# Optimization experiments

Hardware: AMD Instinct MI355X
Metric: run time of the kernel (lower is better)

Reference implementation:

```python
import jax, jax.numpy as jnp
import numpy as np
import math

D_MODEL = 1024
NUM_HEADS = 16
D_K = D_MODEL // NUM_HEADS
THETA = 10000.0
BATCH = 2
SEQ = 2048


def setup_inputs() -> dict:
    key = jax.random.key(0)
    k = jax.random.split(key, 6)
    scale = 1.0 / math.sqrt(D_MODEL)
    in_features = jax.random.normal(k[0], (BATCH, SEQ, D_MODEL), dtype=jnp.float32)
    token_positions = jnp.sort(
        jax.random.randint(k[1], (BATCH, SEQ), 0, SEQ), axis=-1
    ).astype(jnp.int32)
    q_proj_weight = jax.random.normal(k[2], (D_MODEL, D_MODEL), dtype=jnp.float32) * scale
    k_proj_weight = jax.random.normal(k[3], (D_MODEL, D_MODEL), dtype=jnp.float32) * scale
    v_proj_weight = jax.random.normal(k[4], (D_MODEL, D_MODEL), dtype=jnp.float32) * scale
    o_proj_weight = jax.random.normal(k[5], (D_MODEL, D_MODEL), dtype=jnp.float32) * scale
    return {
        "in_features": in_features,
        "token_positions": token_positions,
        "q_proj_weight": q_proj_weight,
        "k_proj_weight": k_proj_weight,
        "v_proj_weight": v_proj_weight,
        "o_proj_weight": o_proj_weight,
    }


def _apply_rope(x, positions):
    # x: [b, h, s, d_k]; positions: [b, s]
    freqs = 1.0 / (THETA ** (jnp.arange(0, D_K, 2, dtype=jnp.float32) / D_K))  # [d_k/2]
    angles = positions[:, None, :, None].astype(jnp.float32) * freqs  # [b,1,s,d_k/2]
    cos, sin = jnp.cos(angles), jnp.sin(angles)
    x1 = x[..., 0::2]
    x2 = x[..., 1::2]
    x1r = x1 * cos - x2 * sin
    x2r = x1 * sin + x2 * cos
    # interleave pairs back: stack on new last axis then flatten
    return jnp.stack([x1r, x2r], axis=-1).reshape(x.shape)


def reference(in_features, token_positions, q_proj_weight, k_proj_weight,
              v_proj_weight, o_proj_weight):
    b, s, _ = in_features.shape
    Q = jnp.einsum('bsi,di->bsd', in_features, q_proj_weight)
    K = jnp.einsum('bsi,di->bsd', in_features, k_proj_weight)
    V = jnp.einsum('bsi,di->bsd', in_features, v_proj_weight)
    # split heads: [b, h, s, d_k]
    def split(x):
        return x.reshape(b, s, NUM_HEADS, D_K).transpose(0, 2, 1, 3)
    Q, K, V = split(Q), split(K), split(V)
    Q = _apply_rope(Q, token_positions)
    K = _apply_rope(K, token_positions)
    scores = jnp.einsum('bhqd,bhkd->bhqk', Q, K) / math.sqrt(D_K)
    causal = jnp.tril(jnp.ones((s, s), dtype=bool))  # allowed positions
    scores = jnp.where(causal[None, None], scores, -jnp.inf)
    weights = jax.nn.softmax(scores, axis=-1)
    head_out = jnp.einsum('bhqk,bhkd->bhqd', weights, V)
    combined = head_out.transpose(0, 2, 1, 3).reshape(b, s, D_MODEL)
    return jnp.einsum('bsd,od->bso', combined, o_proj_weight)
```

## Files before the change

kernel.cpp:

```cpp
#include <hip/hip_runtime.h>
#include <hip/hip_bf16.h>
#include <stdint.h>

#define DMODEL 1024
#define NH 16
#define DKH 64
#define BB 2
#define SS 2048
#define MTOT (BB*SS)

#define BK 32
#define TP 136

using f32x4  = __attribute__((ext_vector_type(4))) float;
using bf16x8 = __attribute__((ext_vector_type(8))) __bf16;

#define GLL(g, l) __builtin_amdgcn_global_load_lds( \
    (const __attribute__((address_space(1))) unsigned int*)(g), \
    (__attribute__((address_space(3))) unsigned int*)(l), 16, 0, 0)

__device__ __forceinline__ unsigned short f2bf(float f) {
  union { float f; uint32_t u; } v; v.f = f;
  uint32_t r = v.u + 0x7FFFu + ((v.u >> 16) & 1u);
  return (unsigned short)(r >> 16);
}

__global__ __launch_bounds__(256) void cvt_all(
    const float* __restrict__ X,
    const float* __restrict__ w0, const float* __restrict__ w1,
    const float* __restrict__ w2, const float* __restrict__ w3,
    unsigned short* __restrict__ Xb,
    unsigned short* __restrict__ Wb)
{
  const int bid = blockIdx.x;
  const float* src;
  unsigned short* dst;
  int i;
  if (bid < 2048) {
    src = X; dst = Xb; i = bid * 256 + threadIdx.x;
  } else {
    int t = bid - 2048;
    int z = t >> 9;
    src = (z == 0) ? w0 : (z == 1) ? w1 : (z == 2) ? w2 : w3;
    dst = Wb + (size_t)z * DMODEL * DMODEL;
    i = (t & 511) * 256 + threadIdx.x;
  }
  const float4* s4 = (const float4*)src;
  float4 a = s4[2*i], b = s4[2*i+1];
  uint4 o;
  o.x = (uint32_t)f2bf(a.x) | ((uint32_t)f2bf(a.y) << 16);
  o.y = (uint32_t)f2bf(a.z) | ((uint32_t)f2bf(a.w) << 16);
  o.z = (uint32_t)f2bf(b.x) | ((uint32_t)f2bf(b.y) << 16);
  o.w = (uint32_t)f2bf(b.z) | ((uint32_t)f2bf(b.w) << 16);
  *(uint4*)(dst + (size_t)i * 8) = o;
}

template<int MI, int NI>
__device__ __forceinline__ void gemm_pipe(
    const unsigned short* __restrict__ A,
    const unsigned short* __restrict__ Bw,
    int m0, int n0, int K,
    unsigned short* As, unsigned short* Bs,
    f32x4 (&acc)[MI][NI])
{
  const int BMl = MI * 32;
  const int BNl = NI * 32;
  const int tid = threadIdx.x;
  const int lane = tid & 63;
  const int w = tid >> 6;
  const int wr = w >> 1, wc = w & 1;
  const int lrow = lane & 15;
  const int g = lane >> 4;

  const f32x4 fzero = {0.f, 0.f, 0.f, 0.f};
  #pragma unroll
  for (int i = 0; i < MI; ++i)
    #pragma unroll
    for (int j = 0; j < NI; ++j)
      acc[i][j] = fzero;

  const int nk = K / BK;

  const unsigned short* aSrc[MI / 2];
  const unsigned short* bSrc[NI / 2];
  int aLds[MI / 2], bLds[NI / 2];
  #pragma unroll
  for (int c = 0; c < MI / 2; ++c) {
    int i = tid + c * 256;
    int row = i >> 2, cc = i & 3;
    int sc = cc ^ ((row >> 1) & 3);
    aSrc[c] = A + (size_t)(m0 + row) * K + sc * 8;
    aLds[c] = i * 8;
  }
  #pragma unroll
  for (int c = 0; c < NI / 2; ++c) {
    int i = tid + c * 256;
    int row = i >> 2, cc = i & 3;
    int sc = cc ^ ((row >> 1) & 3);
    bSrc[c] = Bw + (size_t)(n0 + row) * K + sc * 8;
    bLds[c] = i * 8;
  }
  int aOff[MI], bOff[NI];
  #pragma unroll
  for (int mi = 0; mi < MI; ++mi) {
    int row = wr * (MI * 16) + mi * 16 + lrow;
    aOff[mi] = row * BK + (g ^ ((row >> 1) & 3)) * 8;
  }
  #pragma unroll
  for (int ni = 0; ni < NI; ++ni) {
    int row = wc * (NI * 16) + ni * 16 + lrow;
    bOff[ni] = row * BK + (g ^ ((row >> 1) & 3)) * 8;
  }

  auto STAGE = [&](int k0, int buf) {
    #pragma unroll
    for (int c = 0; c < MI / 2; ++c)
      GLL(aSrc[c] + k0, As + buf * (BMl * BK) + aLds[c]);
    #pragma unroll
    for (int c = 0; c < NI / 2; ++c)
      GLL(bSrc[c] + k0, Bs + buf * (BNl * BK) + bLds[c]);
  };

  STAGE(0, 0);
  __syncthreads();
  for (int t = 0; t < nk; ++t) {
    const int cur = t & 1;
    if (t + 1 < nk) STAGE((t + 1) * BK, cur ^ 1);

    const unsigned short* Ab = As + cur * (BMl * BK);
    const unsigned short* Bb = Bs + cur * (BNl * BK);
    bf16x8 af[MI], bfr[NI];
    #pragma unroll
    for (int mi = 0; mi < MI; ++mi)
      af[mi] = *(const bf16x8*)(Ab + aOff[mi]);
    #pragma unroll
    for (int ni = 0; ni < NI; ++ni)
      bfr[ni] = *(const bf16x8*)(Bb + bOff[ni]);
    #pragma unroll
    for (int mi = 0; mi < MI; ++mi)
      #pragma unroll
      for (int ni = 0; ni < NI; ++ni)
        acc[mi][ni] = __builtin_amdgcn_mfma_f32_16x16x32_bf16(af[mi], bfr[ni], acc[mi][ni], 0, 0, 0);

    __syncthreads();
  }
}

__global__ __launch_bounds__(256) void gemm_qkv(
    const unsigned short* __restrict__ Xb,
    const unsigned short* __restrict__ Wf,
    const int* __restrict__ tpos,
    unsigned short* __restrict__ Qh,
    unsigned short* __restrict__ Kh,
    unsigned short* __restrict__ Vt)
{
  __shared__ __align__(16) unsigned char smraw[128 * TP * 2];
  unsigned short* sm = (unsigned short*)smraw;
  unsigned short* As = sm;
  unsigned short* Bs = sm + 2 * 128 * BK;

  const int m0 = blockIdx.x * 128;
  const int n0 = blockIdx.y * 128;
  const int z  = n0 >> 10;
  const int nloc = n0 & 1023;

  f32x4 acc[4][4];
  gemm_pipe<4, 4>(Xb, Wf, m0, n0, DMODEL, As, Bs, acc);

  const int tid  = threadIdx.x;
  const int lane = tid & 63;
  const int w    = tid >> 6;
  const int wr   = w >> 1, wc = w & 1;
  const int cb   = lane & 15, rb = (lane >> 4) * 4;

  if (z < 2) {
    #pragma unroll
    for (int mi = 0; mi < 4; ++mi)
      #pragma unroll
      for (int ni = 0; ni < 4; ++ni)
        #pragma unroll
        for (int r = 0; r < 4; ++r)
          sm[(wr * 64 + mi * 16 + rb + r) * TP + wc * 64 + ni * 16 + cb] = f2bf(acc[mi][ni][r]);
  } else {
    #pragma unroll
    for (int mi = 0; mi < 4; ++mi)
      #pragma unroll
      for (int ni = 0; ni < 4; ++ni)
        #pragma unroll
        for (int r = 0; r < 4; ++r)
          sm[(wc * 64 + ni * 16 + cb) * TP + wr * 64 + mi * 16 + rb + r] = f2bf(acc[mi][ni][r]);
  }
  __syncthreads();

  const int b = m0 >> 11;
  const float l2t = 13.28771237954945f / 32.0f;
  const float qsc = (z == 0) ? 0.18033688011112042f : 1.0f;

  if (z < 2) {
    unsigned short* dst = (z == 0) ? Qh : Kh;
    #pragma unroll
    for (int p = 0; p < 8; ++p) {
      const int m_l = p * 16 + (tid >> 4);
      const int ck  = tid & 15;
      bf16x8 vals = *(const bf16x8*)(sm + m_l * TP + ck * 8);
      const int m = m0 + m_l, s = m & (SS - 1);
      const int pos = tpos[m];
      const int n = nloc + ck * 8, h = n >> 6, dh = n & 63;
      union { unsigned short u[8]; uint4 v; } ov;
      #pragma unroll
      for (int e = 0; e < 4; ++e) {
        float x1 = (float)vals[2 * e], x2 = (float)vals[2 * e + 1];
        int j = (dh >> 1) + e;
        float ang = (float)pos * exp2f(-(float)j * l2t);
        float sn, cs;
        __sincosf(ang, &sn, &cs);
        sn *= qsc; cs *= qsc;
        ov.u[2 * e]     = f2bf(x1 * cs - x2 * sn);
        ov.u[2 * e + 1] = f2bf(x1 * sn + x2 * cs);
      }
      *(uint4*)(dst + ((size_t)(b * NH + h) * SS + s) * DKH + dh) = ov.v;
    }
  } else {
    #pragma unroll
    for (int p = 0; p < 8; ++p) {
      const int n_l = p * 16 + (tid >> 4);
      const int ck  = tid & 15;
      bf16x8 vals = *(const bf16x8*)(sm + n_l * TP + ck * 8);
      const int n = nloc + n_l, h = n >> 6, dh = n & 63;
      const int m = m0 + ck * 8, s = m & (SS - 1);
      *(bf16x8*)(Vt + ((size_t)(b * NH + h) * DKH + dh) * SS + s) = vals;
    }
  }
}

__global__ __launch_bounds__(256) void attn(
    const unsigned short* __restrict__ Qh,
    const unsigned short* __restrict__ Kh,
    const unsigned short* __restrict__ Vt,
    unsigned short* __restrict__ comb)
{
  __shared__ unsigned short Ks[2][128 * 64];
  __shared__ unsigned short Vs[2][64 * 128];
  __shared__ unsigned short Ps[4][32 * 64];

  const int idx = blockIdx.x;
  const int x = idx & 7;
  const int o = idx >> 3;
  const int bh = x * 4 + (o & 3);
  const int j = o >> 2;
  const int qt = (j < 8) ? j : 23 - j;

  const int tid = threadIdx.x, lane = tid & 63, w = tid >> 6;
  const int lc = lane & 15, lh = lane >> 4;

  const unsigned short* kb = Kh + (size_t)bh * SS * DKH;
  const unsigned short* vb = Vt + (size_t)bh * DKH * SS;
  const int b = bh >> 4, h = bh & 15;
  const f32x4 fzero = {0.f, 0.f, 0.f, 0.f};
  const int Q0 = qt * 128;

  auto STAGE = [&](int t, int buf) {
    const int kv0 = t * 128;
    #pragma unroll
    for (int c = 0; c < 4; ++c) {
      int i = tid + c * 256;
      int row = i >> 3, pc = i & 7;
      int sc = pc ^ (row & 7);
      GLL(kb + (size_t)(kv0 + row) * DKH + sc * 8, &Ks[buf][i * 8]);
    }
    #pragma unroll
    for (int c = 0; c < 4; ++c) {
      int i = tid + c * 256;
      int row = i >> 4, cc = i & 15;
      int sc = cc ^ (row & 7);
      GLL(vb + (size_t)row * SS + kv0 + sc * 8, &Vs[buf][i * 8]);
    }
  };

  bf16x8 qf[2][2];
  #pragma unroll
  for (int qg = 0; qg < 2; ++qg) {
    const unsigned short* Qb = Qh + ((size_t)bh * SS + Q0 + w * 32 + qg * 16 + lc) * DKH;
    qf[qg][0] = *(const bf16x8*)(Qb + lh * 8);
    qf[qg][1] = *(const bf16x8*)(Qb + lh * 8 + 32);
  }

  f32x4 oacc[2][4];
  #pragma unroll
  for (int qg = 0; qg < 2; ++qg)
    #pragma unroll
    for (int i = 0; i < 4; ++i) oacc[qg][i] = fzero;
  float lsum[2] = {0.f, 0.f};
  unsigned short* psw = &Ps[w][0];

  auto QK = [&](int cur, int hh, f32x4 (&sacc)[2][4]) {
    __builtin_amdgcn_s_setprio(1);
    #pragma unroll
    for (int nf = 0; nf < 4; ++nf) {
      const int row = hh * 64 + nf * 16 + lc;
      bf16x8 kf0 = *(const bf16x8*)(&Ks[cur][row * 64 + ((lh) ^ (row & 7)) * 8]);
      bf16x8 kf1 = *(const bf16x8*)(&Ks[cur][row * 64 + ((lh + 4) ^ (row & 7)) * 8]);
      #pragma unroll
      for (int qg = 0; qg < 2; ++qg) {
        sacc[qg][nf] = __builtin_amdgcn_mfma_f32_16x16x32_bf16(kf0, qf[qg][0], fzero, 0, 0, 0);
        sacc[qg][nf] = __builtin_amdgcn_mfma_f32_16x16x32_bf16(kf1, qf[qg][1], sacc[qg][nf], 0, 0, 0);
      }
    }
    __builtin_amdgcn_s_setprio(0);
  };

  auto SM = [&](f32x4 (&sacc)[2][4], bool domask, int t, int hh) {
    #pragma unroll
    for (int qg = 0; qg < 2; ++qg) {
      float sv[4][4];
      if (domask) {
        const int kv0 = t * 128 + hh * 64;
        const int qlane = Q0 + w * 32 + qg * 16 + lc;
        #pragma unroll
        for (int nf = 0; nf < 4; ++nf)
          #pragma unroll
          for (int r = 0; r < 4; ++r) {
            float x2 = sacc[qg][nf][r];
            if ((kv0 + nf * 16 + lh * 4 + r) > qlane) x2 = -1e30f;
            sv[nf][r] = x2;
          }
      } else {
        #pragma unroll
        for (int nf = 0; nf < 4; ++nf)
          #pragma unroll
          for (int r = 0; r < 4; ++r)
            sv[nf][r] = sacc[qg][nf][r];
      }
      float rs = 0.f;
      #pragma unroll
      for (int nf = 0; nf < 4; ++nf)
        #pragma unroll
        for (int r = 0; r < 4; ++r) {
          float p = exp2f(sv[nf][r]);
          sv[nf][r] = p;
          rs += p;
        }
      lsum[qg] += rs;
      #pragma unroll
      for (int nf = 0; nf < 4; ++nf) {
        uint32_t u0, u1;
        asm("v_cvt_pk_bf16_f32 %0, %1, %2" : "=v"(u0) : "v"(sv[nf][0]), "v"(sv[nf][1]));
        asm("v_cvt_pk_bf16_f32 %0, %1, %2" : "=v"(u1) : "v"(sv[nf][2]), "v"(sv[nf][3]));
        int swz = (nf * 2 + (lh >> 1)) ^ (lc & 7);
        uint32_t* p = (uint32_t*)&psw[(qg * 16 + lc) * 64 + swz * 8 + (lh & 1) * 4];
        p[0] = u0; p[1] = u1;
      }
    }
  };

  auto PV = [&](int cur, int hh) {
    __builtin_amdgcn_s_setprio(1);
    #pragma unroll
    for (int c = 0; c < 2; ++c) {
      bf16x8 pf[2];
      #pragma unroll
      for (int qg = 0; qg < 2; ++qg)
        pf[qg] = *(const bf16x8*)(&psw[(qg * 16 + lc) * 64 + ((c * 4 + lh) ^ (lc & 7)) * 8]);
      #pragma unroll
      for (int df = 0; df < 4; ++df) {
        const int row = df * 16 + lc;
        bf16x8 vf = *(const bf16x8*)(&Vs[cur][row * 128 + ((hh * 8 + c * 4 + lh) ^ (row & 7)) * 8]);
        #pragma unroll
        for (int qg = 0; qg < 2; ++qg)
          oacc[qg][df] = __builtin_amdgcn_mfma_f32_16x16x32_bf16(pf[qg], vf, oacc[qg][df], 0, 0, 0);
      }
    }
    __builtin_amdgcn_s_setprio(0);
  };

  STAGE(0, 0);
  for (int t = 0; t < qt; ++t) {
    const int cur = t & 1;
    asm volatile("s_waitcnt vmcnt(0)" ::: "memory");
    __builtin_amdgcn_s_barrier();
    f32x4 sacc[2][4];
    QK(cur, 0, sacc);
    STAGE(t + 1, cur ^ 1);
    SM(sacc, false, t, 0);
    PV(cur, 0);
    QK(cur, 1, sacc);
    SM(sacc, false, t, 1);
    PV(cur, 1);
  }
  {
    const int cur = qt & 1;
    asm volatile("s_waitcnt vmcnt(0)" ::: "memory");
    __builtin_amdgcn_s_barrier();
    f32x4 sacc[2][4];
    QK(cur, 0, sacc);
    SM(sacc, true, qt, 0);
    PV(cur, 0);
    QK(cur, 1, sacc);
    SM(sacc, true, qt, 1);
    PV(cur, 1);
  }

  #pragma unroll
  for (int qg = 0; qg < 2; ++qg) {
    float ls0 = lsum[qg];
    ls0 += __shfl_xor(ls0, 16);
    ls0 += __shfl_xor(ls0, 32);
    #pragma unroll
    for (int r = 0; r < 4; ++r) {
      float ls = __shfl(ls0, lh * 4 + r);
      float inv = 1.f / ls;
      const int q = Q0 + w * 32 + qg * 16 + lh * 4 + r;
      #pragma unroll
      for (int df = 0; df < 4; ++df) {
        const int d = h * 64 + df * 16 + lc;
        comb[((size_t)(b * SS + q)) * DMODEL + d] = f2bf(oacc[qg][df][r] * inv);
      }
    }
  }
}

__global__ __launch_bounds__(256) void gemm_out(
    const unsigned short* __restrict__ Cb,
    const unsigned short* __restrict__ Wob,
    float* __restrict__ out)
{
  __shared__ __align__(16) unsigned char smraw[128 * TP * 2];
  unsigned short* As = (unsigned short*)smraw;
  unsigned short* Bs = (unsigned short*)smraw + 2 * 128 * BK;
  float* smf = (float*)smraw;

  const int m0 = blockIdx.x * 128, n0 = blockIdx.y * 64;
  f32x4 acc[4][2];
  gemm_pipe<4, 2>(Cb, Wob, m0, n0, DMODEL, As, Bs, acc);

  const int tid  = threadIdx.x;
  const int lane = tid & 63;
  const int w    = tid >> 6;
  const int wr   = w >> 1, wc = w & 1;
  const int cb   = lane & 15, rb = (lane >> 4) * 4;

  #pragma unroll
  for (int mi = 0; mi < 4; ++mi)
    #pragma unroll
    for (int ni = 0; ni < 2; ++ni)
      #pragma unroll
      for (int r = 0; r < 4; ++r)
        smf[(wr * 64 + mi * 16 + rb + r) * 68 + wc * 32 + ni * 16 + cb] = acc[mi][ni][r];
  __syncthreads();

  #pragma unroll
  for (int p = 0; p < 8; ++p) {
    const int row = p * 16 + (tid >> 4);
    const int ck  = tid & 15;
    float4 vv = *(const float4*)(smf + row * 68 + ck * 4);
    *(float4*)(out + (size_t)(m0 + row) * DMODEL + n0 + ck * 4) = vv;
  }
}

extern "C" void kernel_launch(void* const* d_in, const int* in_sizes, int n_in,
                              void* d_out, int out_size, void* d_ws, size_t ws_size,
                              hipStream_t stream) {
  (void)in_sizes; (void)n_in; (void)out_size; (void)ws_size;
  const float* X    = (const float*)d_in[0];
  const int*   tpos = (const int*)d_in[1];
  const float* Wq   = (const float*)d_in[2];
  const float* Wk   = (const float*)d_in[3];
  const float* Wv   = (const float*)d_in[4];
  const float* Wo   = (const float*)d_in[5];
  float* out = (float*)d_out;

  uint8_t* ws = (uint8_t*)d_ws;
  const size_t SZ_X = (size_t)MTOT * DMODEL * 2;
  const size_t SZ_W = (size_t)DMODEL * DMODEL * 2;
  const size_t SZ_H = (size_t)BB * NH * SS * DKH * 2;
  unsigned short* Xb   = (unsigned short*)(ws);
  unsigned short* Wqb  = (unsigned short*)(ws + SZ_X);
  unsigned short* Wob  = (unsigned short*)(ws + SZ_X + 3 * SZ_W);
  unsigned short* Qh   = (unsigned short*)(ws + SZ_X + 4 * SZ_W);
  unsigned short* Kh   = (unsigned short*)(ws + SZ_X + 4 * SZ_W + SZ_H);
  unsigned short* Vt   = (unsigned short*)(ws + SZ_X + 4 * SZ_W + 2 * SZ_H);
  unsigned short* comb = Xb;

  cvt_all<<<dim3(4096), dim3(256), 0, stream>>>(X, Wq, Wk, Wv, Wo, Xb, Wqb);

  gemm_qkv<<<dim3(MTOT / 128, 24), dim3(256), 0, stream>>>(Xb, Wqb, tpos, Qh, Kh, Vt);
  attn<<<dim3(512), dim3(256), 0, stream>>>(Qh, Kh, Vt, comb);
  gemm_out<<<dim3(MTOT / 128, 16), dim3(256), 0, stream>>>(comb, Wob, out);
}
```

Measured before the change: 112.4 us.

## Widen QKV GEMM K-tile to 64 and batch both QK halves before softmax

The shared GEMM pipeline gains a K-unroll template parameter. The QKV projection now stages 64-wide K tiles with a new 8-chunk XOR swizzle, which halves the number of barrier and stage iterations at the cost of 64KB of LDS per block. The attention loop now issues both QK sub-tile MFMAs before the prefetch and softmax instead of interleaving them, giving more independent MFMA work per step. The cost is extra score registers and lower occupancy from the larger LDS footprint.

```diff
diff --git a/kernel.cpp b/kernel.cpp
--- a/kernel.cpp
+++ b/kernel.cpp
@@ -9,7 +9,6 @@
 #define SS 2048
 #define MTOT (BB*SS)
 
-#define BK 32
 #define TP 136
 
 using f32x4  = __attribute__((ext_vector_type(4))) float;
@@ -55,7 +54,7 @@
   *(uint4*)(dst + (size_t)i * 8) = o;
 }
 
-template<int MI, int NI>
+template<int MI, int NI, int KU>
 __device__ __forceinline__ void gemm_pipe(
     const unsigned short* __restrict__ A,
     const unsigned short* __restrict__ Bw,
@@ -63,6 +62,7 @@
     unsigned short* As, unsigned short* Bs,
     f32x4 (&acc)[MI][NI])
 {
+  const int BKT = 32 * KU;
   const int BMl = MI * 32;
   const int BNl = NI * 32;
   const int tid = threadIdx.x;
@@ -79,68 +79,78 @@
     for (int j = 0; j < NI; ++j)
       acc[i][j] = fzero;
 
-  const int nk = K / BK;
-
-  const unsigned short* aSrc[MI / 2];
-  const unsigned short* bSrc[NI / 2];
-  int aLds[MI / 2], bLds[NI / 2];
-  #pragma unroll
-  for (int c = 0; c < MI / 2; ++c) {
+  const int nk = K / BKT;
+
+  const unsigned short* aSrc[(MI * KU) / 2];
+  const unsigned short* bSrc[(NI * KU) / 2];
+  int aLds[(MI * KU) / 2], bLds[(NI * KU) / 2];
+  #pragma unroll
+  for (int c = 0; c < (MI * KU) / 2; ++c) {
     int i = tid + c * 256;
-    int row = i >> 2, cc = i & 3;
-    int sc = cc ^ ((row >> 1) & 3);
+    int row, sc;
+    if constexpr (KU == 1) { row = i >> 2; sc = (i & 3) ^ ((row >> 1) & 3); }
+    else                   { row = i >> 3; sc = (i & 7) ^ (row & 7); }
     aSrc[c] = A + (size_t)(m0 + row) * K + sc * 8;
     aLds[c] = i * 8;
   }
   #pragma unroll
-  for (int c = 0; c < NI / 2; ++c) {
+  for (int c = 0; c < (NI * KU) / 2; ++c) {
     int i = tid + c * 256;
-    int row = i >> 2, cc = i & 3;
-    int sc = cc ^ ((row >> 1) & 3);
+    int row, sc;
+    if constexpr (KU == 1) { row = i >> 2; sc = (i & 3) ^ ((row >> 1) & 3); }
+    else                   { row = i >> 3; sc = (i & 7) ^ (row & 7); }
     bSrc[c] = Bw + (size_t)(n0 + row) * K + sc * 8;
     bLds[c] = i * 8;
   }
-  int aOff[MI], bOff[NI];
-  #pragma unroll
-  for (int mi = 0; mi < MI; ++mi) {
-    int row = wr * (MI * 16) + mi * 16 + lrow;
-    aOff[mi] = row * BK + (g ^ ((row >> 1) & 3)) * 8;
-  }
-  #pragma unroll
-  for (int ni = 0; ni < NI; ++ni) {
-    int row = wc * (NI * 16) + ni * 16 + lrow;
-    bOff[ni] = row * BK + (g ^ ((row >> 1) & 3)) * 8;
+  int aOff[KU][MI], bOff[KU][NI];
+  #pragma unroll
+  for (int u = 0; u < KU; ++u) {
+    #pragma unroll
+    for (int mi = 0; mi < MI; ++mi) {
+      int row = wr * (MI * 16) + mi * 16 + lrow;
+      int ch = (KU == 1) ? (g ^ ((row >> 1) & 3)) : ((g + 4 * u) ^ (row & 7));
+      aOff[u][mi] = row * BKT + ch * 8;
+    }
+    #pragma unroll
+    for (int ni = 0; ni < NI; ++ni) {
+      int row = wc * (NI * 16) + ni * 16 + lrow;
+      int ch = (KU == 1) ? (g ^ ((row >> 1) & 3)) : ((g + 4 * u) ^ (row & 7));
+      bOff[u][ni] = row * BKT + ch * 8;
+    }
   }
 
   auto STAGE = [&](int k0, int buf) {
     #pragma unroll
-    for (int c = 0; c < MI / 2; ++c)
-      GLL(aSrc[c] + k0, As + buf * (BMl * BK) + aLds[c]);
-    #pragma unroll
-    for (int c = 0; c < NI / 2; ++c)
-      GLL(bSrc[c] + k0, Bs + buf * (BNl * BK) + bLds[c]);
+    for (int c = 0; c < (MI * KU) / 2; ++c)
+      GLL(aSrc[c] + k0, As + buf * (BMl * BKT) + aLds[c]);
+    #pragma unroll
+    for (int c = 0; c < (NI * KU) / 2; ++c)
+      GLL(bSrc[c] + k0, Bs + buf * (BNl * BKT) + bLds[c]);
   };
 
   STAGE(0, 0);
   __syncthreads();
   for (int t = 0; t < nk; ++t) {
     const int cur = t & 1;
-    if (t + 1 < nk) STAGE((t + 1) * BK, cur ^ 1);
-
-    const unsigned short* Ab = As + cur * (BMl * BK);
-    const unsigned short* Bb = Bs + cur * (BNl * BK);
-    bf16x8 af[MI], bfr[NI];
-    #pragma unroll
-    for (int mi = 0; mi < MI; ++mi)
-      af[mi] = *(const bf16x8*)(Ab + aOff[mi]);
-    #pragma unroll
-    for (int ni = 0; ni < NI; ++ni)
-      bfr[ni] = *(const bf16x8*)(Bb + bOff[ni]);
-    #pragma unroll
-    for (int mi = 0; mi < MI; ++mi)
+    if (t + 1 < nk) STAGE((t + 1) * BKT, cur ^ 1);
+
+    const unsigned short* Ab = As + cur * (BMl * BKT);
+    const unsigned short* Bb = Bs + cur * (BNl * BKT);
+    #pragma unroll
+    for (int u = 0; u < KU; ++u) {
+      bf16x8 af[MI], bfr[NI];
+      #pragma unroll
+      for (int mi = 0; mi < MI; ++mi)
+        af[mi] = *(const bf16x8*)(Ab + aOff[u][mi]);
       #pragma unroll
       for (int ni = 0; ni < NI; ++ni)
-        acc[mi][ni] = __builtin_amdgcn_mfma_f32_16x16x32_bf16(af[mi], bfr[ni], acc[mi][ni], 0, 0, 0);
+        bfr[ni] = *(const bf16x8*)(Bb + bOff[u][ni]);
+      #pragma unroll
+      for (int mi = 0; mi < MI; ++mi)
+        #pragma unroll
+        for (int ni = 0; ni < NI; ++ni)
+          acc[mi][ni] = __builtin_amdgcn_mfma_f32_16x16x32_bf16(af[mi], bfr[ni], acc[mi][ni], 0, 0, 0);
+    }
 
     __syncthreads();
   }
@@ -154,10 +164,10 @@
     unsigned short* __restrict__ Kh,
     unsigned short* __restrict__ Vt)
 {
-  __shared__ __align__(16) unsigned char smraw[128 * TP * 2];
+  __shared__ __align__(16) unsigned char smraw[65536];
   unsigned short* sm = (unsigned short*)smraw;
   unsigned short* As = sm;
-  unsigned short* Bs = sm + 2 * 128 * BK;
+  unsigned short* Bs = sm + 2 * 128 * 64;
 
   const int m0 = blockIdx.x * 128;
   const int n0 = blockIdx.y * 128;
@@ -165,7 +175,7 @@
   const int nloc = n0 & 1023;
 
   f32x4 acc[4][4];
-  gemm_pipe<4, 4>(Xb, Wf, m0, n0, DMODEL, As, Bs, acc);
+  gemm_pipe<4, 4, 2>(Xb, Wf, m0, n0, DMODEL, As, Bs, acc);
 
   const int tid  = threadIdx.x;
   const int lane = tid & 63;
@@ -378,25 +388,25 @@
     const int cur = t & 1;
     asm volatile("s_waitcnt vmcnt(0)" ::: "memory");
     __builtin_amdgcn_s_barrier();
-    f32x4 sacc[2][4];
-    QK(cur, 0, sacc);
+    f32x4 sA[2][4], sB[2][4];
+    QK(cur, 0, sA);
+    QK(cur, 1, sB);
     STAGE(t + 1, cur ^ 1);
-    SM(sacc, false, t, 0);
+    SM(sA, false, t, 0);
     PV(cur, 0);
-    QK(cur, 1, sacc);
-    SM(sacc, false, t, 1);
+    SM(sB, false, t, 1);
     PV(cur, 1);
   }
   {
     const int cur = qt & 1;
     asm volatile("s_waitcnt vmcnt(0)" ::: "memory");
     __builtin_amdgcn_s_barrier();
-    f32x4 sacc[2][4];
-    QK(cur, 0, sacc);
-    SM(sacc, true, qt, 0);
+    f32x4 sA[2][4], sB[2][4];
+    QK(cur, 0, sA);
+    QK(cur, 1, sB);
+    SM(sA, true, qt, 0);
     PV(cur, 0);
-    QK(cur, 1, sacc);
-    SM(sacc, true, qt, 1);
+    SM(sB, true, qt, 1);
     PV(cur, 1);
   }
 
@@ -426,12 +436,12 @@
 {
   __shared__ __align__(16) unsigned char smraw[128 * TP * 2];
   unsigned short* As = (unsigned short*)smraw;
-  unsigned short* Bs = (unsigned short*)smraw + 2 * 128 * BK;
+  unsigned short* Bs = (unsigned short*)smraw + 2 * 128 * 32;
   float* smf = (float*)smraw;
 
   const int m0 = blockIdx.x * 128, n0 = blockIdx.y * 64;
   f32x4 acc[4][2];
-  gemm_pipe<4, 2>(Cb, Wob, m0, n0, DMODEL, As, Bs, acc);
+  gemm_pipe<4, 2, 1>(Cb, Wob, m0, n0, DMODEL, As, Bs, acc);
 
   const int tid  = threadIdx.x;
   const int lane = tid & 63;
```

Result: faster. 104.8 us (-6.8%).
